# Performance work log

Measured on AMD Instinct MI355X. Metric: run time of the kernel, lower is better.

Reference implementation:

```python
import jax, jax.numpy as jnp
import numpy as np

LOG2_HASHMAP_SIZE = 19
HASHTABLE_SIZE = 2 ** LOG2_HASHMAP_SIZE
FEATURES_PER_LEVEL = 2
RES = 128
N_POINTS = 4194304

# Instant-NGP spatial hash primes (prime0 = 1)
_P1 = jnp.uint32(2654435761)
_P2 = jnp.uint32(805459861)


def _hash3(ix, iy, iz):
    # uint32 wrap-around multiply/xor matches torch int32 overflow bit pattern;
    # modulus is a power of two, so uint32 mod == floored int32 mod low bits.
    h = ix.astype(jnp.uint32) ^ (iy.astype(jnp.uint32) * _P1) ^ (iz.astype(jnp.uint32) * _P2)
    return (h % jnp.uint32(HASHTABLE_SIZE)).astype(jnp.int32)


def setup_inputs() -> dict:
    key = jax.random.key(0)
    kx, kt = jax.random.split(key)
    x = jax.random.uniform(kx, (N_POINTS, 3), dtype=jnp.float32)
    # hashtable = rand*2-1, scaled by hashmap_scale (=1)
    hashtable = jax.random.uniform(kt, (HASHTABLE_SIZE, FEATURES_PER_LEVEL), dtype=jnp.float32) * 2.0 - 1.0
    return {"x": x, "hashtable": hashtable}


def reference(x, hashtable):
    xr = x.reshape(-1, 3)
    x_scaled = xr * RES
    xf = jnp.floor(x_scaled).astype(jnp.int32)   # [N,3]
    xc = jnp.ceil(x_scaled).astype(jnp.int32)    # [N,3]

    fx, fy, fz = xf[:, 0], xf[:, 1], xf[:, 2]
    cx, cy, cz = xc[:, 0], xc[:, 1], xc[:, 2]

    # 8 corner hashes, ordering matches (h0..h7) = (000,100,010,001,110,101,011,111)
    h000 = _hash3(fx, fy, fz)
    h100 = _hash3(cx, fy, fz)
    h010 = _hash3(fx, cy, fz)
    h001 = _hash3(fx, fy, cz)
    h110 = _hash3(cx, cy, fz)
    h101 = _hash3(cx, fy, cz)
    h011 = _hash3(fx, cy, cz)
    h111 = _hash3(cx, cy, cz)

    idx = jnp.stack([h000, h100, h010, h001, h110, h101, h011, h111], axis=0)  # [8,N]
    v = hashtable[idx]  # [8, N, F] scattered gather
    v000, v100, v010, v001, v110, v101, v011, v111 = v

    d = x_scaled - xf.astype(x_scaled.dtype)  # [N,3] fractional offsets
    dx = d[:, 0:1]
    dy = d[:, 1:2]
    dz = d[:, 2:3]

    c00 = v000 * (1 - dx) + v100 * dx
    c01 = v001 * (1 - dx) + v101 * dx
    c10 = v010 * (1 - dx) + v110 * dx
    c11 = v011 * (1 - dx) + v111 * dx
    c0 = c00 * (1 - dy) + c10 * dy
    c1 = c01 * (1 - dy) + c11 * dy
    out = c0 * (1 - dz) + c1 * dz  # [N, F]

    return out.reshape(x.shape[:-1] + (FEATURES_PER_LEVEL,))
```

## Files before the change

kernel.cpp:

```cpp
#include <hip/hip_runtime.h>
#include <stdint.h>

#define LOG2_HASHMAP_SIZE 19
#define HASHTABLE_SIZE (1u << LOG2_HASHMAP_SIZE)
#define HASHTABLE_MASK (HASHTABLE_SIZE - 1u)
#define RES_F 128.0f

typedef float f32x2 __attribute__((ext_vector_type(2)));
typedef float f32x4 __attribute__((ext_vector_type(4)));
typedef uint32_t u32x4 __attribute__((ext_vector_type(4)));
typedef int i32x4 __attribute__((ext_vector_type(4)));

__device__ u32x4 llvm_amdgcn_raw_buffer_load_v4u32(i32x4 rsrc, int voffset,
                                                   int soffset, int aux)
    __asm("llvm.amdgcn.raw.buffer.load.v4i32");
__device__ uint32_t llvm_amdgcn_raw_buffer_load_u32(i32x4 rsrc, int voffset,
                                                    int soffset, int aux)
    __asm("llvm.amdgcn.raw.buffer.load.i32");

__device__ __forceinline__ i32x4 make_srd(const void* p, uint32_t bytes) {
    union { const void* p; uint32_t u[2]; } a;
    a.p = p;
    i32x4 r;
    r.x = (int)a.u[0];
    r.y = (int)(a.u[1] & 0xFFFFu);
    r.z = (int)bytes;
    r.w = 0x00020000;
    return r;
}

__device__ __forceinline__ f32x2 nt_load2(const f32x2* p) {
    return __builtin_nontemporal_load(p);
}
__device__ __forceinline__ void nt_store4(f32x4* p, f32x4 v) {
    __builtin_nontemporal_store(v, p);
}

__device__ __forceinline__ float bf16w_lo(uint32_t w) {
    return __uint_as_float(w << 16);
}
__device__ __forceinline__ float bf16w_hi(uint32_t w) {
    return __uint_as_float(w & 0xFFFF0000u);
}

__device__ __forceinline__ uint32_t sel4(u32x4 q, uint32_t e) {
    uint32_t lo = (e & 1u) ? q.y : q.x;
    uint32_t hi = (e & 1u) ? q.w : q.z;
    return (e & 2u) ? hi : lo;
}

__device__ __forceinline__ uint32_t pack_bf16x2(float a, float b) {
    uint32_t ua = __float_as_uint(a);
    uint32_t ub = __float_as_uint(b);
    ua = ua + 0x7FFFu + ((ua >> 16) & 1u);
    ub = ub + 0x7FFFu + ((ub >> 16) & 1u);
    return (ua >> 16) | (ub & 0xFFFF0000u);
}

__global__ __launch_bounds__(256) void convert_table_kernel(
    const f32x4* __restrict__ table4,
    u32x4* __restrict__ ws4)
{
    int i = blockIdx.x * blockDim.x + threadIdx.x;
    f32x4 e01 = table4[2 * i + 0];
    f32x4 e23 = table4[2 * i + 1];
    u32x4 o;
    o.x = pack_bf16x2(e01.x, e01.y);
    o.y = pack_bf16x2(e01.z, e01.w);
    o.z = pack_bf16x2(e23.x, e23.y);
    o.w = pack_bf16x2(e23.z, e23.w);
    ws4[i] = o;
}

__global__ __launch_bounds__(256, 8) void featurefield_bf16_kernel(
    const f32x2* __restrict__ x2,
    const uint32_t* __restrict__ tb,
    f32x4* __restrict__ out4,
    int n_pairs)
{
    int t = blockIdx.x * blockDim.x + threadIdx.x;
    if (t >= n_pairs) return;

    i32x4 srd = make_srd(tb, HASHTABLE_SIZE * 4u);

    f32x2 A = nt_load2(&x2[3 * t + 0]);
    f32x2 B = nt_load2(&x2[3 * t + 1]);
    f32x2 C = nt_load2(&x2[3 * t + 2]);

    float px[2] = {A.x, B.y};
    float py[2] = {A.y, C.x};
    float pz[2] = {B.x, C.y};

    uint32_t i0[2][4];
    uint32_t mm[2];
    float dxs[2], dys[2], dzs[2];

    #pragma unroll
    for (int k = 0; k < 2; ++k) {
        float xs = px[k] * RES_F;
        float ys = py[k] * RES_F;
        float zs = pz[k] * RES_F;
        float fxf = floorf(xs), fyf = floorf(ys), fzf = floorf(zs);
        int fx = (int)fxf, fy = (int)fyf, fz = (int)fzf;
        int cx = (int)ceilf(xs), cy = (int)ceilf(ys), cz = (int)ceilf(zs);
        dxs[k] = xs - fxf;
        dys[k] = ys - fyf;
        dzs[k] = zs - fzf;

        uint32_t ufx = (uint32_t)fx;
        mm[k] = ufx ^ (uint32_t)cx;
        uint32_t fyp = (uint32_t)fy * 2654435761u;
        uint32_t cyp = (uint32_t)cy * 2654435761u;
        uint32_t fzp = (uint32_t)fz * 805459861u;
        uint32_t czp = (uint32_t)cz * 805459861u;

        i0[k][0] = (ufx ^ fyp ^ fzp) & HASHTABLE_MASK;
        i0[k][1] = (ufx ^ cyp ^ fzp) & HASHTABLE_MASK;
        i0[k][2] = (ufx ^ fyp ^ czp) & HASHTABLE_MASK;
        i0[k][3] = (ufx ^ cyp ^ czp) & HASHTABLE_MASK;
    }

    u32x4 q[2][4];
    #pragma unroll
    for (int k = 0; k < 2; ++k) {
        #pragma unroll
        for (int j = 0; j < 4; ++j) {
            q[k][j] = llvm_amdgcn_raw_buffer_load_v4u32(
                srd, (int)((i0[k][j] << 2) & ~15u), 0, 0);
        }
    }

    uint32_t w0[2][4], w1[2][4];
    #pragma unroll
    for (int k = 0; k < 2; ++k) {
        #pragma unroll
        for (int j = 0; j < 4; ++j) {
            uint32_t e0 = i0[k][j] & 3u;
            w0[k][j] = sel4(q[k][j], e0);
            w1[k][j] = sel4(q[k][j], e0 ^ (mm[k] & 3u));
        }
        if (mm[k] > 3u) {
            #pragma unroll
            for (int j = 0; j < 4; ++j) {
                w1[k][j] = llvm_amdgcn_raw_buffer_load_u32(
                    srd, (int)((i0[k][j] ^ mm[k]) << 2), 0, 0);
            }
        }
    }

    f32x2 res[2];
    #pragma unroll
    for (int k = 0; k < 2; ++k) {
        float dx = dxs[k], dy = dys[k], dz = dzs[k];
        float wx = 1.0f - dx, wy = 1.0f - dy, wz = 1.0f - dz;

        float c00x = bf16w_lo(w0[k][0]) * wx + bf16w_lo(w1[k][0]) * dx;
        float c00y = bf16w_hi(w0[k][0]) * wx + bf16w_hi(w1[k][0]) * dx;
        float c10x = bf16w_lo(w0[k][1]) * wx + bf16w_lo(w1[k][1]) * dx;
        float c10y = bf16w_hi(w0[k][1]) * wx + bf16w_hi(w1[k][1]) * dx;
        float c01x = bf16w_lo(w0[k][2]) * wx + bf16w_lo(w1[k][2]) * dx;
        float c01y = bf16w_hi(w0[k][2]) * wx + bf16w_hi(w1[k][2]) * dx;
        float c11x = bf16w_lo(w0[k][3]) * wx + bf16w_lo(w1[k][3]) * dx;
        float c11y = bf16w_hi(w0[k][3]) * wx + bf16w_hi(w1[k][3]) * dx;

        float c0x = c00x * wy + c10x * dy;
        float c0y = c00y * wy + c10y * dy;
        float c1x = c01x * wy + c11x * dy;
        float c1y = c01y * wy + c11y * dy;

        res[k].x = c0x * wz + c1x * dz;
        res[k].y = c0y * wz + c1y * dz;
    }

    f32x4 o = {res[0].x, res[0].y, res[1].x, res[1].y};
    nt_store4(&out4[t], o);
}

__global__ __launch_bounds__(256) void featurefield_fp32_kernel(
    const f32x2* __restrict__ x2,
    const float2* __restrict__ table,
    f32x4* __restrict__ out4,
    int n_pairs)
{
    int t = blockIdx.x * blockDim.x + threadIdx.x;
    if (t >= n_pairs) return;

    f32x2 A = nt_load2(&x2[3 * t + 0]);
    f32x2 B = nt_load2(&x2[3 * t + 1]);
    f32x2 C = nt_load2(&x2[3 * t + 2]);

    float px[2] = {A.x, B.y};
    float py[2] = {A.y, C.x};
    float pz[2] = {B.x, C.y};

    f32x2 res[2];
    #pragma unroll
    for (int k = 0; k < 2; ++k) {
        float xs = px[k] * RES_F, ys = py[k] * RES_F, zs = pz[k] * RES_F;
        float fxf = floorf(xs), fyf = floorf(ys), fzf = floorf(zs);
        int fx = (int)fxf, fy = (int)fyf, fz = (int)fzf;
        int cx = (int)ceilf(xs), cy = (int)ceilf(ys), cz = (int)ceilf(zs);
        float dx = xs - fxf, dy = ys - fyf, dz = zs - fzf;
        uint32_t ufx = (uint32_t)fx, ucx = (uint32_t)cx;
        uint32_t fyp = (uint32_t)fy * 2654435761u, cyp = (uint32_t)cy * 2654435761u;
        uint32_t fzp = (uint32_t)fz * 805459861u, czp = (uint32_t)cz * 805459861u;
        uint32_t h0 = (ufx ^ fyp ^ fzp) & HASHTABLE_MASK;
        uint32_t h1 = (ucx ^ fyp ^ fzp) & HASHTABLE_MASK;
        uint32_t h2 = (ufx ^ cyp ^ fzp) & HASHTABLE_MASK;
        uint32_t h3 = (ufx ^ fyp ^ czp) & HASHTABLE_MASK;
        uint32_t h4 = (ucx ^ cyp ^ fzp) & HASHTABLE_MASK;
        uint32_t h5 = (ucx ^ fyp ^ czp) & HASHTABLE_MASK;
        uint32_t h6 = (ufx ^ cyp ^ czp) & HASHTABLE_MASK;
        uint32_t h7 = (ucx ^ cyp ^ czp) & HASHTABLE_MASK;

        float2 v0 = table[h0], v1 = table[h1], v2 = table[h2], v3 = table[h3];
        float2 v4 = table[h4], v5 = table[h5], v6 = table[h6], v7 = table[h7];

        float wx = 1.0f - dx, wy = 1.0f - dy, wz = 1.0f - dz;
        float c00x = v0.x * wx + v1.x * dx, c00y = v0.y * wx + v1.y * dx;
        float c01x = v3.x * wx + v5.x * dx, c01y = v3.y * wx + v5.y * dx;
        float c10x = v2.x * wx + v4.x * dx, c10y = v2.y * wx + v4.y * dx;
        float c11x = v6.x * wx + v7.x * dx, c11y = v6.y * wx + v7.y * dx;
        float c0x = c00x * wy + c10x * dy, c0y = c00y * wy + c10y * dy;
        float c1x = c01x * wy + c11x * dy, c1y = c01y * wy + c11y * dy;
        res[k].x = c0x * wz + c1x * dz;
        res[k].y = c0y * wz + c1y * dz;
    }

    f32x4 o = {res[0].x, res[0].y, res[1].x, res[1].y};
    nt_store4(&out4[t], o);
}

extern "C" void kernel_launch(void* const* d_in, const int* in_sizes, int n_in,
                              void* d_out, int out_size, void* d_ws, size_t ws_size,
                              hipStream_t stream) {
    const f32x2* x2 = (const f32x2*)d_in[0];
    f32x4* out4 = (f32x4*)d_out;

    int n_points = in_sizes[0] / 3;
    int n_pairs = n_points / 2;
    int block = 256;
    int grid = (n_pairs + block - 1) / block;

    size_t need = (size_t)HASHTABLE_SIZE * 4u;
    if (ws_size >= need) {
        const f32x4* table4 = (const f32x4*)d_in[1];
        u32x4* ws4 = (u32x4*)d_ws;
        int conv_threads = HASHTABLE_SIZE / 4;
        convert_table_kernel<<<conv_threads / 256, 256, 0, stream>>>(table4, ws4);
        featurefield_bf16_kernel<<<grid, block, 0, stream>>>(
            x2, (const uint32_t*)d_ws, out4, n_pairs);
    } else {
        const float2* table = (const float2*)d_in[1];
        featurefield_fp32_kernel<<<grid, block, 0, stream>>>(x2, table, out4, n_pairs);
    }
}
```

Baseline: 178.4 us.

## Software-pipeline four strided points per thread to overlap gathers with interpolation

Each thread now handles four points spaced NT apart instead of two adjacent points. The issue and consume phases are interleaved, so the table gathers for the next point are in flight while the current one is interpolated. Input loads become scalar strided-by-thread loads, which coalesce across a wavefront, and each output is an 8-byte store rather than a 16-byte store. The aim is more memory-level parallelism per thread; the cost is higher register pressure, a quarter as many threads, and dropping the occupancy hint from the launch bounds.

```diff
diff --git a/kernel.cpp b/kernel.cpp
--- a/kernel.cpp
+++ b/kernel.cpp
@@ -27,13 +27,6 @@
     r.z = (int)bytes;
     r.w = 0x00020000;
     return r;
-}
-
-__device__ __forceinline__ f32x2 nt_load2(const f32x2* p) {
-    return __builtin_nontemporal_load(p);
-}
-__device__ __forceinline__ void nt_store4(f32x4* p, f32x4 v) {
-    __builtin_nontemporal_store(v, p);
 }
 
 __device__ __forceinline__ float bf16w_lo(uint32_t w) {
@@ -72,186 +65,180 @@
     ws4[i] = o;
 }
 
-__global__ __launch_bounds__(256, 8) void featurefield_bf16_kernel(
-    const f32x2* __restrict__ x2,
+
+struct Gen {
+    u32x4 q[4];
+    uint32_t w1[4];
+    uint32_t i0[4];
+    uint32_t mm;
+    float dx, dy, dz;
+};
+
+__device__ __forceinline__ Gen issue_point(const float* __restrict__ x,
+                                           i32x4 srd, int p) {
+    Gen g;
+    float xs = __builtin_nontemporal_load(x + 3 * p + 0) * RES_F;
+    float ys = __builtin_nontemporal_load(x + 3 * p + 1) * RES_F;
+    float zs = __builtin_nontemporal_load(x + 3 * p + 2) * RES_F;
+    float fxf = floorf(xs), fyf = floorf(ys), fzf = floorf(zs);
+    int fx = (int)fxf, fy = (int)fyf, fz = (int)fzf;
+    int cx = (int)ceilf(xs), cy = (int)ceilf(ys), cz = (int)ceilf(zs);
+    g.dx = xs - fxf;
+    g.dy = ys - fyf;
+    g.dz = zs - fzf;
+
+    uint32_t ufx = (uint32_t)fx;
+    g.mm = ufx ^ (uint32_t)cx;
+    uint32_t fyp = (uint32_t)fy * 2654435761u;
+    uint32_t cyp = (uint32_t)cy * 2654435761u;
+    uint32_t fzp = (uint32_t)fz * 805459861u;
+    uint32_t czp = (uint32_t)cz * 805459861u;
+
+    g.i0[0] = (ufx ^ fyp ^ fzp) & HASHTABLE_MASK;
+    g.i0[1] = (ufx ^ cyp ^ fzp) & HASHTABLE_MASK;
+    g.i0[2] = (ufx ^ fyp ^ czp) & HASHTABLE_MASK;
+    g.i0[3] = (ufx ^ cyp ^ czp) & HASHTABLE_MASK;
+
+    #pragma unroll
+    for (int j = 0; j < 4; ++j) {
+        g.q[j] = llvm_amdgcn_raw_buffer_load_v4u32(
+            srd, (int)((g.i0[j] << 2) & ~15u), 0, 0);
+    }
+    if (g.mm > 3u) {
+        #pragma unroll
+        for (int j = 0; j < 4; ++j) {
+            g.w1[j] = llvm_amdgcn_raw_buffer_load_u32(
+                srd, (int)((g.i0[j] ^ g.mm) << 2), 0, 0);
+        }
+    }
+    return g;
+}
+
+__device__ __forceinline__ f32x2 consume_point(const Gen& g) {
+    uint32_t w0[4], w1[4];
+    #pragma unroll
+    for (int j = 0; j < 4; ++j) {
+        uint32_t e0 = g.i0[j] & 3u;
+        w0[j] = sel4(g.q[j], e0);
+        w1[j] = (g.mm <= 3u) ? sel4(g.q[j], e0 ^ g.mm) : g.w1[j];
+    }
+
+    float dx = g.dx, dy = g.dy, dz = g.dz;
+    float wx = 1.0f - dx, wy = 1.0f - dy, wz = 1.0f - dz;
+
+    float c00x = bf16w_lo(w0[0]) * wx + bf16w_lo(w1[0]) * dx;
+    float c00y = bf16w_hi(w0[0]) * wx + bf16w_hi(w1[0]) * dx;
+    float c10x = bf16w_lo(w0[1]) * wx + bf16w_lo(w1[1]) * dx;
+    float c10y = bf16w_hi(w0[1]) * wx + bf16w_hi(w1[1]) * dx;
+    float c01x = bf16w_lo(w0[2]) * wx + bf16w_lo(w1[2]) * dx;
+    float c01y = bf16w_hi(w0[2]) * wx + bf16w_hi(w1[2]) * dx;
+    float c11x = bf16w_lo(w0[3]) * wx + bf16w_lo(w1[3]) * dx;
+    float c11y = bf16w_hi(w0[3]) * wx + bf16w_hi(w1[3]) * dx;
+
+    float c0x = c00x * wy + c10x * dy;
+    float c0y = c00y * wy + c10y * dy;
+    float c1x = c01x * wy + c11x * dy;
+    float c1y = c01y * wy + c11y * dy;
+
+    f32x2 r;
+    r.x = c0x * wz + c1x * dz;
+    r.y = c0y * wz + c1y * dz;
+    return r;
+}
+
+__device__ __forceinline__ void store_out(f32x2* __restrict__ out, int p,
+                                          f32x2 v) {
+    __builtin_nontemporal_store(v, out + p);
+}
+
+__global__ __launch_bounds__(256) void featurefield_pipe_kernel(
+    const float* __restrict__ x,
     const uint32_t* __restrict__ tb,
-    f32x4* __restrict__ out4,
-    int n_pairs)
+    f32x2* __restrict__ out,
+    int NT)
 {
     int t = blockIdx.x * blockDim.x + threadIdx.x;
-    if (t >= n_pairs) return;
+    if (t >= NT) return;
 
     i32x4 srd = make_srd(tb, HASHTABLE_SIZE * 4u);
 
-    f32x2 A = nt_load2(&x2[3 * t + 0]);
-    f32x2 B = nt_load2(&x2[3 * t + 1]);
-    f32x2 C = nt_load2(&x2[3 * t + 2]);
-
-    float px[2] = {A.x, B.y};
-    float py[2] = {A.y, C.x};
-    float pz[2] = {B.x, C.y};
-
-    uint32_t i0[2][4];
-    uint32_t mm[2];
-    float dxs[2], dys[2], dzs[2];
-
-    #pragma unroll
-    for (int k = 0; k < 2; ++k) {
-        float xs = px[k] * RES_F;
-        float ys = py[k] * RES_F;
-        float zs = pz[k] * RES_F;
-        float fxf = floorf(xs), fyf = floorf(ys), fzf = floorf(zs);
-        int fx = (int)fxf, fy = (int)fyf, fz = (int)fzf;
-        int cx = (int)ceilf(xs), cy = (int)ceilf(ys), cz = (int)ceilf(zs);
-        dxs[k] = xs - fxf;
-        dys[k] = ys - fyf;
-        dzs[k] = zs - fzf;
-
-        uint32_t ufx = (uint32_t)fx;
-        mm[k] = ufx ^ (uint32_t)cx;
-        uint32_t fyp = (uint32_t)fy * 2654435761u;
-        uint32_t cyp = (uint32_t)cy * 2654435761u;
-        uint32_t fzp = (uint32_t)fz * 805459861u;
-        uint32_t czp = (uint32_t)cz * 805459861u;
-
-        i0[k][0] = (ufx ^ fyp ^ fzp) & HASHTABLE_MASK;
-        i0[k][1] = (ufx ^ cyp ^ fzp) & HASHTABLE_MASK;
-        i0[k][2] = (ufx ^ fyp ^ czp) & HASHTABLE_MASK;
-        i0[k][3] = (ufx ^ cyp ^ czp) & HASHTABLE_MASK;
-    }
-
-    u32x4 q[2][4];
-    #pragma unroll
-    for (int k = 0; k < 2; ++k) {
-        #pragma unroll
-        for (int j = 0; j < 4; ++j) {
-            q[k][j] = llvm_amdgcn_raw_buffer_load_v4u32(
-                srd, (int)((i0[k][j] << 2) & ~15u), 0, 0);
-        }
-    }
-
-    uint32_t w0[2][4], w1[2][4];
-    #pragma unroll
-    for (int k = 0; k < 2; ++k) {
-        #pragma unroll
-        for (int j = 0; j < 4; ++j) {
-            uint32_t e0 = i0[k][j] & 3u;
-            w0[k][j] = sel4(q[k][j], e0);
-            w1[k][j] = sel4(q[k][j], e0 ^ (mm[k] & 3u));
-        }
-        if (mm[k] > 3u) {
-            #pragma unroll
-            for (int j = 0; j < 4; ++j) {
-                w1[k][j] = llvm_amdgcn_raw_buffer_load_u32(
-                    srd, (int)((i0[k][j] ^ mm[k]) << 2), 0, 0);
-            }
-        }
-    }
-
-    f32x2 res[2];
-    #pragma unroll
-    for (int k = 0; k < 2; ++k) {
-        float dx = dxs[k], dy = dys[k], dz = dzs[k];
-        float wx = 1.0f - dx, wy = 1.0f - dy, wz = 1.0f - dz;
-
-        float c00x = bf16w_lo(w0[k][0]) * wx + bf16w_lo(w1[k][0]) * dx;
-        float c00y = bf16w_hi(w0[k][0]) * wx + bf16w_hi(w1[k][0]) * dx;
-        float c10x = bf16w_lo(w0[k][1]) * wx + bf16w_lo(w1[k][1]) * dx;
-        float c10y = bf16w_hi(w0[k][1]) * wx + bf16w_hi(w1[k][1]) * dx;
-        float c01x = bf16w_lo(w0[k][2]) * wx + bf16w_lo(w1[k][2]) * dx;
-        float c01y = bf16w_hi(w0[k][2]) * wx + bf16w_hi(w1[k][2]) * dx;
-        float c11x = bf16w_lo(w0[k][3]) * wx + bf16w_lo(w1[k][3]) * dx;
-        float c11y = bf16w_hi(w0[k][3]) * wx + bf16w_hi(w1[k][3]) * dx;
-
-        float c0x = c00x * wy + c10x * dy;
-        float c0y = c00y * wy + c10y * dy;
-        float c1x = c01x * wy + c11x * dy;
-        float c1y = c01y * wy + c11y * dy;
-
-        res[k].x = c0x * wz + c1x * dz;
-        res[k].y = c0y * wz + c1y * dz;
-    }
-
-    f32x4 o = {res[0].x, res[0].y, res[1].x, res[1].y};
-    nt_store4(&out4[t], o);
+    Gen g0 = issue_point(x, srd, t);
+    Gen g1 = issue_point(x, srd, t + NT);
+    store_out(out, t, consume_point(g0));
+    Gen g2 = issue_point(x, srd, t + 2 * NT);
+    store_out(out, t + NT, consume_point(g1));
+    Gen g3 = issue_point(x, srd, t + 3 * NT);
+    store_out(out, t + 2 * NT, consume_point(g2));
+    store_out(out, t + 3 * NT, consume_point(g3));
 }
 
 __global__ __launch_bounds__(256) void featurefield_fp32_kernel(
-    const f32x2* __restrict__ x2,
+    const float* __restrict__ x,
     const float2* __restrict__ table,
-    f32x4* __restrict__ out4,
-    int n_pairs)
+    f32x2* __restrict__ out,
+    int n_points)
 {
-    int t = blockIdx.x * blockDim.x + threadIdx.x;
-    if (t >= n_pairs) return;
-
-    f32x2 A = nt_load2(&x2[3 * t + 0]);
-    f32x2 B = nt_load2(&x2[3 * t + 1]);
-    f32x2 C = nt_load2(&x2[3 * t + 2]);
-
-    float px[2] = {A.x, B.y};
-    float py[2] = {A.y, C.x};
-    float pz[2] = {B.x, C.y};
-
-    f32x2 res[2];
-    #pragma unroll
-    for (int k = 0; k < 2; ++k) {
-        float xs = px[k] * RES_F, ys = py[k] * RES_F, zs = pz[k] * RES_F;
-        float fxf = floorf(xs), fyf = floorf(ys), fzf = floorf(zs);
-        int fx = (int)fxf, fy = (int)fyf, fz = (int)fzf;
-        int cx = (int)ceilf(xs), cy = (int)ceilf(ys), cz = (int)ceilf(zs);
-        float dx = xs - fxf, dy = ys - fyf, dz = zs - fzf;
-        uint32_t ufx = (uint32_t)fx, ucx = (uint32_t)cx;
-        uint32_t fyp = (uint32_t)fy * 2654435761u, cyp = (uint32_t)cy * 2654435761u;
-        uint32_t fzp = (uint32_t)fz * 805459861u, czp = (uint32_t)cz * 805459861u;
-        uint32_t h0 = (ufx ^ fyp ^ fzp) & HASHTABLE_MASK;
-        uint32_t h1 = (ucx ^ fyp ^ fzp) & HASHTABLE_MASK;
-        uint32_t h2 = (ufx ^ cyp ^ fzp) & HASHTABLE_MASK;
-        uint32_t h3 = (ufx ^ fyp ^ czp) & HASHTABLE_MASK;
-        uint32_t h4 = (ucx ^ cyp ^ fzp) & HASHTABLE_MASK;
-        uint32_t h5 = (ucx ^ fyp ^ czp) & HASHTABLE_MASK;
-        uint32_t h6 = (ufx ^ cyp ^ czp) & HASHTABLE_MASK;
-        uint32_t h7 = (ucx ^ cyp ^ czp) & HASHTABLE_MASK;
-
-        float2 v0 = table[h0], v1 = table[h1], v2 = table[h2], v3 = table[h3];
-        float2 v4 = table[h4], v5 = table[h5], v6 = table[h6], v7 = table[h7];
-
-        float wx = 1.0f - dx, wy = 1.0f - dy, wz = 1.0f - dz;
-        float c00x = v0.x * wx + v1.x * dx, c00y = v0.y * wx + v1.y * dx;
-        float c01x = v3.x * wx + v5.x * dx, c01y = v3.y * wx + v5.y * dx;
-        float c10x = v2.x * wx + v4.x * dx, c10y = v2.y * wx + v4.y * dx;
-        float c11x = v6.x * wx + v7.x * dx, c11y = v6.y * wx + v7.y * dx;
-        float c0x = c00x * wy + c10x * dy, c0y = c00y * wy + c10y * dy;
-        float c1x = c01x * wy + c11x * dy, c1y = c01y * wy + c11y * dy;
-        res[k].x = c0x * wz + c1x * dz;
-        res[k].y = c0y * wz + c1y * dz;
-    }
-
-    f32x4 o = {res[0].x, res[0].y, res[1].x, res[1].y};
-    nt_store4(&out4[t], o);
+    int p = blockIdx.x * blockDim.x + threadIdx.x;
+    if (p >= n_points) return;
+
+    float xs = x[3 * p + 0] * RES_F;
+    float ys = x[3 * p + 1] * RES_F;
+    float zs = x[3 * p + 2] * RES_F;
+    float fxf = floorf(xs), fyf = floorf(ys), fzf = floorf(zs);
+    int fx = (int)fxf, fy = (int)fyf, fz = (int)fzf;
+    int cx = (int)ceilf(xs), cy = (int)ceilf(ys), cz = (int)ceilf(zs);
+    float dx = xs - fxf, dy = ys - fyf, dz = zs - fzf;
+    uint32_t ufx = (uint32_t)fx, ucx = (uint32_t)cx;
+    uint32_t fyp = (uint32_t)fy * 2654435761u, cyp = (uint32_t)cy * 2654435761u;
+    uint32_t fzp = (uint32_t)fz * 805459861u, czp = (uint32_t)cz * 805459861u;
+    uint32_t h0 = (ufx ^ fyp ^ fzp) & HASHTABLE_MASK;
+    uint32_t h1 = (ucx ^ fyp ^ fzp) & HASHTABLE_MASK;
+    uint32_t h2 = (ufx ^ cyp ^ fzp) & HASHTABLE_MASK;
+    uint32_t h3 = (ufx ^ fyp ^ czp) & HASHTABLE_MASK;
+    uint32_t h4 = (ucx ^ cyp ^ fzp) & HASHTABLE_MASK;
+    uint32_t h5 = (ucx ^ fyp ^ czp) & HASHTABLE_MASK;
+    uint32_t h6 = (ufx ^ cyp ^ czp) & HASHTABLE_MASK;
+    uint32_t h7 = (ucx ^ cyp ^ czp) & HASHTABLE_MASK;
+
+    float2 v0 = table[h0], v1 = table[h1], v2 = table[h2], v3 = table[h3];
+    float2 v4 = table[h4], v5 = table[h5], v6 = table[h6], v7 = table[h7];
+
+    float wx = 1.0f - dx, wy = 1.0f - dy, wz = 1.0f - dz;
+    float c00x = v0.x * wx + v1.x * dx, c00y = v0.y * wx + v1.y * dx;
+    float c01x = v3.x * wx + v5.x * dx, c01y = v3.y * wx + v5.y * dx;
+    float c10x = v2.x * wx + v4.x * dx, c10y = v2.y * wx + v4.y * dx;
+    float c11x = v6.x * wx + v7.x * dx, c11y = v6.y * wx + v7.y * dx;
+    float c0x = c00x * wy + c10x * dy, c0y = c00y * wy + c10y * dy;
+    float c1x = c01x * wy + c11x * dy, c1y = c01y * wy + c11y * dy;
+
+    f32x2 r;
+    r.x = c0x * wz + c1x * dz;
+    r.y = c0y * wz + c1y * dz;
+    __builtin_nontemporal_store(r, out + p);
 }
 
 extern "C" void kernel_launch(void* const* d_in, const int* in_sizes, int n_in,
                               void* d_out, int out_size, void* d_ws, size_t ws_size,
                               hipStream_t stream) {
-    const f32x2* x2 = (const f32x2*)d_in[0];
-    f32x4* out4 = (f32x4*)d_out;
+    const float* x = (const float*)d_in[0];
+    f32x2* out = (f32x2*)d_out;
 
     int n_points = in_sizes[0] / 3;
-    int n_pairs = n_points / 2;
-    int block = 256;
-    int grid = (n_pairs + block - 1) / block;
-
     size_t need = (size_t)HASHTABLE_SIZE * 4u;
-    if (ws_size >= need) {
+
+    if (ws_size >= need && (n_points & 3) == 0) {
         const f32x4* table4 = (const f32x4*)d_in[1];
         u32x4* ws4 = (u32x4*)d_ws;
         int conv_threads = HASHTABLE_SIZE / 4;
         convert_table_kernel<<<conv_threads / 256, 256, 0, stream>>>(table4, ws4);
-        featurefield_bf16_kernel<<<grid, block, 0, stream>>>(
-            x2, (const uint32_t*)d_ws, out4, n_pairs);
+
+        int NT = n_points / 4;
+        int grid = (NT + 255) / 256;
+        featurefield_pipe_kernel<<<grid, 256, 0, stream>>>(
+            x, (const uint32_t*)d_ws, out, NT);
     } else {
         const float2* table = (const float2*)d_in[1];
-        featurefield_fp32_kernel<<<grid, block, 0, stream>>>(x2, table, out4, n_pairs);
-    }
-}
+        int grid = (n_points + 255) / 256;
+        featurefield_fp32_kernel<<<grid, 256, 0, stream>>>(x, table, out, n_points);
+    }
+}
```

Result: no change. 179.8 us (+0.8%).
